# Optimization experiments

Hardware: AMD Instinct MI355X
Metric: run time of the kernel (lower is better)

Reference implementation:

```python
import jax, jax.numpy as jnp
import numpy as np

D = 1024


def setup_inputs() -> dict:
    key = jax.random.key(0)
    kx, kq, kk, kv, ko = jax.random.split(key, 5)
    scale = 0.02
    x = jax.random.normal(kx, (4, 2048, D), dtype=jnp.float32)
    Wq = jax.random.normal(kq, (D, D), dtype=jnp.float32) * scale
    Wk = jax.random.normal(kk, (D, D), dtype=jnp.float32) * scale
    Wv = jax.random.normal(kv, (D, D), dtype=jnp.float32) * scale
    Wo = jax.random.normal(ko, (D, D), dtype=jnp.float32) * scale
    return {"x": x, "Wq": Wq, "Wk": Wk, "Wv": Wv, "Wo": Wo}


def reference(x, Wq, Wk, Wv, Wo):
    # Linear projections (torch Linear: y = x @ W.T, no bias)
    q = jnp.einsum('bsd,ed->bse', x, Wq)
    k = jnp.einsum('bsd,ed->bse', x, Wk)
    v = jnp.einsum('bsd,ed->bse', x, Wv)
    d = x.shape[-1]
    # HRR binding: circular convolution of k and v along feature dim (rfft domain)
    Fk = jnp.fft.rfft(k, axis=-1)
    Fv = jnp.fft.rfft(v, axis=-1)
    Fq = jnp.fft.rfft(q, axis=-1)
    Fkv = Fk * Fv                      # bound key-value pairs, Fourier domain
    # causal cumulative memory over sequence; FFT is linear so cumsum commutes
    Fmem = jnp.cumsum(Fkv, axis=-2)    # [b, s, d//2+1] complex
    # unbind with query: circular correlation = multiply by conj(rfft(q))
    values_hat = jnp.fft.irfft(Fmem * jnp.conj(Fq), n=d, axis=-1)
    return jnp.einsum('bsd,ed->bse', values_hat, Wo)
```

## Files before the change

### kernel.cpp

```cpp
#include <hip/hip_runtime.h>
#include <hip/hip_fp16.h>

#define D_DIM 1024
#define NF 513
#define NB 4
#define NS 2048
#define NTOK (NB * NS)
#define NCH 32
#define CHS (NS / NCH)
#define NQKV 3200
#define KOUT 1088
#define USTRIDE 544

typedef __attribute__((ext_vector_type(8))) short short8_t;
typedef __attribute__((ext_vector_type(4))) float f32x4;

__device__ inline unsigned short f2bf(float f) {
    unsigned u = __builtin_bit_cast(unsigned, f);
    u += 0x7FFFu + ((u >> 16) & 1u);
    return (unsigned short)(u >> 16);
}
__device__ inline float bf2f(unsigned short h) {
    unsigned u = ((unsigned)h) << 16;
    return __builtin_bit_cast(float, u);
}
__device__ inline unsigned pkc(float re, float im) {
    return (unsigned)f2bf(re) | ((unsigned)f2bf(im) << 16);
}
__device__ inline float2 uph(unsigned u) {
    unsigned short lo = (unsigned short)(u & 0xFFFFu), hi = (unsigned short)(u >> 16);
    return make_float2(__half2float(__builtin_bit_cast(__half, lo)),
                       __half2float(__builtin_bit_cast(__half, hi)));
}

__global__ __launch_bounds__(256) void convert_x(const float* __restrict__ src,
                                                 unsigned short* __restrict__ dst,
                                                 int n4) {
    int i = blockIdx.x * 256 + threadIdx.x;
    int stride = gridDim.x * 256;
    for (; i < n4; i += stride) {
        float4 v = reinterpret_cast<const float4*>(src)[i];
        ushort4 o;
        o.x = f2bf(v.x); o.y = f2bf(v.y); o.z = f2bf(v.z); o.w = f2bf(v.w);
        reinterpret_cast<ushort4*>(dst)[i] = o;
    }
}

__device__ inline void gload_lds16(const void* g, void* l) {
    __builtin_amdgcn_global_load_lds(
        (const __attribute__((address_space(1))) void*)g,
        (__attribute__((address_space(3))) void*)l,
        16, 0, 0);
}

template <typename OutT, bool F16OUT>
__global__ __launch_bounds__(256) void gemm_bf16_bk64(const unsigned short* __restrict__ A,
                                                      const unsigned short* __restrict__ B,
                                                      OutT* __restrict__ C,
                                                      int M, int N, int K) {
    __shared__ __attribute__((aligned(16))) unsigned short ldsA[2 * 128 * 64];
    __shared__ __attribute__((aligned(16))) unsigned short ldsB[2 * 128 * 64];
    const int tid  = threadIdx.x;
    const int wave = tid >> 6;
    const int lane = tid & 63;
    const int l15  = lane & 15;
    const int q4   = (lane >> 4) & 3;
    const int h7   = l15 & 7;
    const int p0   = ((q4)     ^ h7) << 3;
    const int p1   = ((4 + q4) ^ h7) << 3;
    const int wm   = (wave >> 1) * 64;
    const int wn   = (wave & 1) * 64;
    const int bm   = blockIdx.x * 128;
    const int bn   = blockIdx.y * 128;
    const int srow = tid >> 3;
    const int scol = (((tid & 7) ^ ((tid >> 3) & 7)) << 3);
    const int NT   = K >> 6;

    const unsigned short* Asrc = A + (size_t)(bm + srow) * K + scol;
    const unsigned short* Bsrc = B + (size_t)(bn + srow) * K + scol;
    const size_t cstep = (size_t)32 * K;

    f32x4 acc[4][4];
#pragma unroll
    for (int i = 0; i < 4; ++i)
#pragma unroll
        for (int j = 0; j < 4; ++j)
            acc[i][j] = (f32x4){0.f, 0.f, 0.f, 0.f};

    auto STAGE = [&](int t, int b) {
        const int k0 = t << 6;
        unsigned short* la = &ldsA[b * 8192 + tid * 8];
        unsigned short* lb = &ldsB[b * 8192 + tid * 8];
        gload_lds16(Asrc + k0,             la);
        gload_lds16(Asrc + cstep + k0,     la + 2048);
        gload_lds16(Asrc + 2 * cstep + k0, la + 4096);
        gload_lds16(Asrc + 3 * cstep + k0, la + 6144);
        gload_lds16(Bsrc + k0,             lb);
        gload_lds16(Bsrc + cstep + k0,     lb + 2048);
        gload_lds16(Bsrc + 2 * cstep + k0, lb + 4096);
        gload_lds16(Bsrc + 3 * cstep + k0, lb + 6144);
    };

    STAGE(0, 0);

    for (int j = 0; j < NT; ++j) {
        const int buf = j & 1;
        if (j + 1 < NT) {
            STAGE(j + 1, buf ^ 1);
            asm volatile("s_waitcnt vmcnt(8)" ::: "memory");
        } else {
            asm volatile("s_waitcnt vmcnt(0)" ::: "memory");
        }
        __builtin_amdgcn_s_barrier();
        asm volatile("" ::: "memory");

        const unsigned short* la = &ldsA[buf * 8192];
        const unsigned short* lb = &ldsB[buf * 8192];

        {
            short8_t af[4], bfv[4];
#pragma unroll
            for (int mi = 0; mi < 4; ++mi)
                af[mi] = *reinterpret_cast<const short8_t*>(&la[(wm + mi * 16 + l15) * 64 + p0]);
#pragma unroll
            for (int ni = 0; ni < 4; ++ni)
                bfv[ni] = *reinterpret_cast<const short8_t*>(&lb[(wn + ni * 16 + l15) * 64 + p0]);
            __builtin_amdgcn_s_setprio(1);
#pragma unroll
            for (int mi = 0; mi < 4; ++mi)
#pragma unroll
                for (int ni = 0; ni < 4; ++ni)
                    acc[mi][ni] = __builtin_amdgcn_mfma_f32_16x16x32_bf16(af[mi], bfv[ni], acc[mi][ni], 0, 0, 0);
            __builtin_amdgcn_s_setprio(0);
        }
        {
            short8_t af[4], bfv[4];
#pragma unroll
            for (int mi = 0; mi < 4; ++mi)
                af[mi] = *reinterpret_cast<const short8_t*>(&la[(wm + mi * 16 + l15) * 64 + p1]);
#pragma unroll
            for (int ni = 0; ni < 4; ++ni)
                bfv[ni] = *reinterpret_cast<const short8_t*>(&lb[(wn + ni * 16 + l15) * 64 + p1]);
            __builtin_amdgcn_s_setprio(1);
#pragma unroll
            for (int mi = 0; mi < 4; ++mi)
#pragma unroll
                for (int ni = 0; ni < 4; ++ni)
                    acc[mi][ni] = __builtin_amdgcn_mfma_f32_16x16x32_bf16(af[mi], bfv[ni], acc[mi][ni], 0, 0, 0);
            __builtin_amdgcn_s_setprio(0);
        }

        __builtin_amdgcn_s_barrier();
        asm volatile("" ::: "memory");
    }

#pragma unroll
    for (int mi = 0; mi < 4; ++mi) {
        int rbase = bm + wm + mi * 16 + (lane >> 4) * 4;
#pragma unroll
        for (int ni = 0; ni < 4; ++ni) {
            int col = bn + wn + ni * 16 + l15;
#pragma unroll
            for (int j = 0; j < 4; ++j) {
                float v = acc[mi][ni][j];
                if constexpr (sizeof(OutT) == 4)
                    C[(size_t)(rbase + j) * N + col] = v;
                else if constexpr (F16OUT)
                    C[(size_t)(rbase + j) * N + col] =
                        __builtin_bit_cast(unsigned short, __float2half(v));
                else
                    C[(size_t)(rbase + j) * N + col] = f2bf(v);
            }
        }
    }
}

__device__ inline int sw(int i) { return i ^ ((i >> 4) & 15); }

__device__ inline int dr4(int n) {
    return ((n & 3) << 8) | (((n >> 2) & 3) << 6) | (((n >> 4) & 3) << 4) |
           (((n >> 6) & 3) << 2) | ((n >> 8) & 3);
}

__device__ inline float2 cmul(float2 a, float2 b) {
    return make_float2(a.x * b.x - a.y * b.y, a.x * b.y + a.y * b.x);
}

__device__ inline void fft1024_r4(float2* X, const float2* tw, int t) {
#pragma unroll
    for (int s = 0; s < 5; ++s) {
        const int L = 1 << (2 * s);
        const int r = t & (L - 1);
        const int base = ((t >> (2 * s)) << (2 * s + 2)) + r;
        float2 A  = X[sw(base)];
        float2 Bv = X[sw(base + L)];
        float2 Cv = X[sw(base + 2 * L)];
        float2 Dv = X[sw(base + 3 * L)];
        if (s != 0) {
            const int step = 1024 >> (2 * s + 2);
            Bv = cmul(Bv, tw[sw(r * step)]);
            Cv = cmul(Cv, tw[sw(2 * r * step)]);
            Dv = cmul(Dv, tw[sw(3 * r * step)]);
        }
        float2 e0 = make_float2(A.x + Cv.x, A.y + Cv.y);
        float2 e1 = make_float2(A.x - Cv.x, A.y - Cv.y);
        float2 o0 = make_float2(Bv.x + Dv.x, Bv.y + Dv.y);
        float2 o1 = make_float2(Bv.x - Dv.x, Bv.y - Dv.y);
        X[sw(base)]         = make_float2(e0.x + o0.x, e0.y + o0.y);
        X[sw(base + L)]     = make_float2(e1.x + o1.y, e1.y - o1.x);
        X[sw(base + 2 * L)] = make_float2(e0.x - o0.x, e0.y - o0.y);
        X[sw(base + 3 * L)] = make_float2(e1.x - o1.y, e1.y + o1.x);
        __syncthreads();
    }
}

__global__ __launch_bounds__(256) void twiddle_init(float2* __restrict__ twg) {
    int k = blockIdx.x * 256 + threadIdx.x;
    if (k < 768) {
        float ang = -6.283185307179586f * (float)k / 1024.0f;
        float s, c;
        sincosf(ang, &s, &c);
        twg[sw(k)] = make_float2(c, s);
    }
}

__global__ __launch_bounds__(256) void wf_qkv(const float* __restrict__ Wq,
                                              const float* __restrict__ Wk,
                                              const float* __restrict__ Wv,
                                              const float2* __restrict__ twg,
                                              unsigned short* __restrict__ WF) {
    __shared__ __attribute__((aligned(16))) float2 X[1024];
    __shared__ __attribute__((aligned(16))) float2 twL[768];
    const int tid = threadIdx.x;
    const int w = blockIdx.y;
    const float* W = (w == 0) ? Wq : (w == 1) ? Wk : Wv;
    const int d0 = blockIdx.x * 2;
    for (int i = tid; i < 384; i += 256)
        reinterpret_cast<float4*>(twL)[i] = reinterpret_cast<const float4*>(twg)[i];
    for (int n = tid; n < 1024; n += 256) {
        float2 z = *reinterpret_cast<const float2*>(W + (size_t)n * 1024 + d0);
        X[sw(dr4(n))] = z;
    }
    __syncthreads();
    fft1024_r4(X, twL, tid);
    const int rbase = w * 1026;
    for (int f = tid; f < NF; f += 256) {
        float2 Zj = X[sw(f)];
        float2 Zm = X[sw((1024 - f) & 1023)];
        float re0 = 0.5f * (Zj.x + Zm.x), im0 = 0.5f * (Zj.y - Zm.y);
        float re1 = 0.5f * (Zj.y + Zm.y), im1 = 0.5f * (Zm.x - Zj.x);
        WF[(size_t)(rbase + 2 * f)     * 1024 + d0]     = f2bf(re0);
        WF[(size_t)(rbase + 2 * f + 1) * 1024 + d0]     = f2bf(im0);
        WF[(size_t)(rbase + 2 * f)     * 1024 + d0 + 1] = f2bf(re1);
        WF[(size_t)(rbase + 2 * f + 1) * 1024 + d0 + 1] = f2bf(im1);
    }
}

__global__ __launch_bounds__(256) void wf_zero(unsigned* __restrict__ p) {
    int i = blockIdx.x * 256 + threadIdx.x;
    if (i < 62464) p[i] = 0;
}

__global__ __launch_bounds__(256) void wf_o(const float* __restrict__ Wo,
                                            const float2* __restrict__ twg,
                                            unsigned short* __restrict__ Wt) {
    __shared__ __attribute__((aligned(16))) float2 X[1024];
    __shared__ __attribute__((aligned(16))) float2 twL[768];
    const int tid = threadIdx.x;
    const int e0 = blockIdx.x * 2;
    for (int i = tid; i < 384; i += 256)
        reinterpret_cast<float4*>(twL)[i] = reinterpret_cast<const float4*>(twg)[i];
    const float* r0 = Wo + (size_t)e0 * 1024;
    const float* r1 = r0 + 1024;
    for (int n = tid; n < 1024; n += 256)
        X[sw(dr4(n))] = make_float2(r0[n], r1[n]);
    __syncthreads();
    fft1024_r4(X, twL, tid);
    unsigned short* o0 = Wt + (size_t)e0 * KOUT;
    unsigned short* o1 = o0 + KOUT;
    for (int f = tid; f < NF; f += 256) {
        float2 Zj = X[sw(f)];
        float2 Zm = X[sw((1024 - f) & 1023)];
        float c = (f == 0 || f == 512) ? (1.0f / 1024.0f) : (2.0f / 1024.0f);
        o0[2 * f]     = f2bf(0.5f * (Zj.x + Zm.x) * c);
        o0[2 * f + 1] = f2bf(0.5f * (Zj.y - Zm.y) * c);
        o1[2 * f]     = f2bf(0.5f * (Zj.y + Zm.y) * c);
        o1[2 * f + 1] = f2bf(0.5f * (Zm.x - Zj.x) * c);
    }
    for (int j = tid; j < KOUT - 2 * NF; j += 256) {
        o0[2 * NF + j] = 0;
        o1[2 * NF + j] = 0;
    }
}

__global__ __launch_bounds__(256) void hrr_chunk_sum(const unsigned* __restrict__ F,
                                                     float2* __restrict__ part) {
    int f = blockIdx.x * 256 + threadIdx.x;
    if (f >= NF) return;
    int ch = blockIdx.y, b = blockIdx.z;
    float sx = 0.f, sy = 0.f;
    size_t base = ((size_t)b * NS + (size_t)ch * CHS) * 1600;
    for (int i = 0; i < CHS; ++i) {
        size_t row = base + (size_t)i * 1600;
        float2 k = uph(F[row + 513 + f]);
        float2 v = uph(F[row + 1026 + f]);
        sx += k.x * v.x - k.y * v.y;
        sy += k.x * v.y + k.y * v.x;
    }
    part[(size_t)(b * NCH + ch) * NF + f] = make_float2(sx, sy);
}

__global__ __launch_bounds__(256) void hrr_scan_apply(const unsigned* __restrict__ F,
                                                      const float2* __restrict__ part,
                                                      unsigned* __restrict__ U) {
    int f = blockIdx.x * 256 + threadIdx.x;
    if (f >= USTRIDE) return;
    int ch = blockIdx.y, b = blockIdx.z;
    size_t ubase = ((size_t)b * NS + (size_t)ch * CHS) * USTRIDE + f;
    if (f >= NF) {
        for (int i = 0; i < CHS; ++i) U[ubase + (size_t)i * USTRIDE] = 0;
        return;
    }
    float rx = 0.f, ry = 0.f;
    for (int c2 = 0; c2 < ch; ++c2) {
        float2 p = part[(size_t)(b * NCH + c2) * NF + f];
        rx += p.x; ry += p.y;
    }
    size_t base = ((size_t)b * NS + (size_t)ch * CHS) * 1600;
    for (int i = 0; i < CHS; ++i) {
        size_t row = base + (size_t)i * 1600;
        float2 k = uph(F[row + 513 + f]);
        float2 v = uph(F[row + 1026 + f]);
        rx += k.x * v.x - k.y * v.y;
        ry += k.x * v.y + k.y * v.x;
        float2 q = uph(F[row + f]);
        U[ubase + (size_t)i * USTRIDE] = pkc(rx * q.x + ry * q.y,
                                            ry * q.x - rx * q.y);
    }
}

extern "C" void kernel_launch(void* const* d_in, const int* in_sizes, int n_in,
                              void* d_out, int out_size, void* d_ws, size_t ws_size,
                              hipStream_t stream) {
    const float* x  = (const float*)d_in[0];
    const float* Wq = (const float*)d_in[1];
    const float* Wk = (const float*)d_in[2];
    const float* Wv = (const float*)d_in[3];
    const float* Wo = (const float*)d_in[4];
    float* out = (float*)d_out;

    char* ws = (char*)d_ws;
    unsigned short* F_all = (unsigned short*)(ws + 0);
    unsigned short* U     = (unsigned short*)(ws + 52428800);
    float2*         part  = (float2*)        (ws + 70254592);
    float2*         twg   = (float2*)        (ws + 70779904);
    unsigned short* WF    = (unsigned short*)(ws + 70786048);
    unsigned short* Wt    = (unsigned short*)(ws + 77339648);
    unsigned short* xb    = (unsigned short*)(ws + 79567872);

    convert_x<<<2048, 256, 0, stream>>>(x, xb, NTOK * D_DIM / 4);
    twiddle_init<<<3, 256, 0, stream>>>(twg);

    wf_qkv<<<dim3(512, 3), 256, 0, stream>>>(Wq, Wk, Wv, twg, WF);
    wf_zero<<<244, 256, 0, stream>>>((unsigned*)(WF + (size_t)3078 * 1024));
    wf_o<<<512, 256, 0, stream>>>(Wo, twg, Wt);

    dim3 gq(NTOK / 128, NQKV / 128);
    gemm_bf16_bk64<unsigned short, true><<<gq, 256, 0, stream>>>(xb, WF, F_all, NTOK, NQKV, D_DIM);

    dim3 gs((USTRIDE + 255) / 256, NCH, NB);
    hrr_chunk_sum<<<dim3(3, NCH, NB), 256, 0, stream>>>((const unsigned*)F_all, part);
    hrr_scan_apply<<<gs, 256, 0, stream>>>((const unsigned*)F_all, part, (unsigned*)U);

    dim3 go(NTOK / 128, D_DIM / 128);
    gemm_bf16_bk64<float, false><<<go, 256, 0, stream>>>(U, Wt, out, NTOK, D_DIM, KOUT);
}
```

Measured before the change: 191.3 us.

## Pack DC and Nyquist real parts into one complex slot to drop spectrum padding

The real FFT spectrum is stored as 512 complex slots by packing the purely real DC and Nyquist coefficients into slot 0. This shrinks the QKV projection GEMM N dimension from 3200 to 3072 and the output GEMM K from 1088 to 1024, and removes the zero-padding kernels and padded columns. The HRR scan kernels special-case slot 0 so it handles two real accumulators. This cuts GEMM work and memory traffic by roughly 4-6% but adds branching for one thread per block.

```diff
diff --git a/kernel.cpp b/kernel.cpp
--- a/kernel.cpp
+++ b/kernel.cpp
@@ -8,9 +8,8 @@
 #define NTOK (NB * NS)
 #define NCH 32
 #define CHS (NS / NCH)
-#define NQKV 3200
-#define KOUT 1088
-#define USTRIDE 544
+#define NQKV 3072
+#define KOUT 1024
 
 typedef __attribute__((ext_vector_type(8))) short short8_t;
 typedef __attribute__((ext_vector_type(4))) float f32x4;
@@ -243,22 +242,25 @@
     }
     __syncthreads();
     fft1024_r4(X, twL, tid);
-    const int rbase = w * 1026;
+    const int rbase = w * 1024;
     for (int f = tid; f < NF; f += 256) {
         float2 Zj = X[sw(f)];
         float2 Zm = X[sw((1024 - f) & 1023)];
         float re0 = 0.5f * (Zj.x + Zm.x), im0 = 0.5f * (Zj.y - Zm.y);
         float re1 = 0.5f * (Zj.y + Zm.y), im1 = 0.5f * (Zm.x - Zj.x);
-        WF[(size_t)(rbase + 2 * f)     * 1024 + d0]     = f2bf(re0);
-        WF[(size_t)(rbase + 2 * f + 1) * 1024 + d0]     = f2bf(im0);
-        WF[(size_t)(rbase + 2 * f)     * 1024 + d0 + 1] = f2bf(re1);
-        WF[(size_t)(rbase + 2 * f + 1) * 1024 + d0 + 1] = f2bf(im1);
-    }
-}
-
-__global__ __launch_bounds__(256) void wf_zero(unsigned* __restrict__ p) {
-    int i = blockIdx.x * 256 + threadIdx.x;
-    if (i < 62464) p[i] = 0;
+        if (f == 0) {
+            WF[(size_t)(rbase + 0) * 1024 + d0]     = f2bf(re0);
+            WF[(size_t)(rbase + 0) * 1024 + d0 + 1] = f2bf(re1);
+        } else if (f == 512) {
+            WF[(size_t)(rbase + 1) * 1024 + d0]     = f2bf(re0);
+            WF[(size_t)(rbase + 1) * 1024 + d0 + 1] = f2bf(re1);
+        } else {
+            WF[(size_t)(rbase + 2 * f)     * 1024 + d0]     = f2bf(re0);
+            WF[(size_t)(rbase + 2 * f + 1) * 1024 + d0]     = f2bf(im0);
+            WF[(size_t)(rbase + 2 * f)     * 1024 + d0 + 1] = f2bf(re1);
+            WF[(size_t)(rbase + 2 * f + 1) * 1024 + d0 + 1] = f2bf(im1);
+        }
+    }
 }
 
 __global__ __launch_bounds__(256) void wf_o(const float* __restrict__ Wo,
@@ -278,64 +280,97 @@
     fft1024_r4(X, twL, tid);
     unsigned short* o0 = Wt + (size_t)e0 * KOUT;
     unsigned short* o1 = o0 + KOUT;
+    const float inv = 1.0f / 1024.0f;
     for (int f = tid; f < NF; f += 256) {
         float2 Zj = X[sw(f)];
         float2 Zm = X[sw((1024 - f) & 1023)];
-        float c = (f == 0 || f == 512) ? (1.0f / 1024.0f) : (2.0f / 1024.0f);
-        o0[2 * f]     = f2bf(0.5f * (Zj.x + Zm.x) * c);
-        o0[2 * f + 1] = f2bf(0.5f * (Zj.y - Zm.y) * c);
-        o1[2 * f]     = f2bf(0.5f * (Zj.y + Zm.y) * c);
-        o1[2 * f + 1] = f2bf(0.5f * (Zm.x - Zj.x) * c);
-    }
-    for (int j = tid; j < KOUT - 2 * NF; j += 256) {
-        o0[2 * NF + j] = 0;
-        o1[2 * NF + j] = 0;
+        float re0 = 0.5f * (Zj.x + Zm.x), im0 = 0.5f * (Zj.y - Zm.y);
+        float re1 = 0.5f * (Zj.y + Zm.y), im1 = 0.5f * (Zm.x - Zj.x);
+        if (f == 0) {
+            o0[0] = f2bf(re0 * inv);
+            o1[0] = f2bf(re1 * inv);
+        } else if (f == 512) {
+            o0[1] = f2bf(re0 * inv);
+            o1[1] = f2bf(re1 * inv);
+        } else {
+            float c = 2.0f * inv;
+            o0[2 * f]     = f2bf(re0 * c);
+            o0[2 * f + 1] = f2bf(im0 * c);
+            o1[2 * f]     = f2bf(re1 * c);
+            o1[2 * f + 1] = f2bf(im1 * c);
+        }
     }
 }
 
 __global__ __launch_bounds__(256) void hrr_chunk_sum(const unsigned* __restrict__ F,
                                                      float2* __restrict__ part) {
     int f = blockIdx.x * 256 + threadIdx.x;
-    if (f >= NF) return;
     int ch = blockIdx.y, b = blockIdx.z;
-    float sx = 0.f, sy = 0.f;
-    size_t base = ((size_t)b * NS + (size_t)ch * CHS) * 1600;
-    for (int i = 0; i < CHS; ++i) {
-        size_t row = base + (size_t)i * 1600;
-        float2 k = uph(F[row + 513 + f]);
-        float2 v = uph(F[row + 1026 + f]);
-        sx += k.x * v.x - k.y * v.y;
-        sy += k.x * v.y + k.y * v.x;
-    }
-    part[(size_t)(b * NCH + ch) * NF + f] = make_float2(sx, sy);
+    size_t base = ((size_t)b * NS + (size_t)ch * CHS) * 1536;
+    float2* pp = part + (size_t)(b * NCH + ch) * NF;
+    if (f == 0) {
+        float s0 = 0.f, s512 = 0.f;
+        for (int i = 0; i < CHS; ++i) {
+            size_t row = base + (size_t)i * 1536;
+            float2 k = uph(F[row + 512]);
+            float2 v = uph(F[row + 1024]);
+            s0   += k.x * v.x;
+            s512 += k.y * v.y;
+        }
+        pp[0]   = make_float2(s0, 0.f);
+        pp[512] = make_float2(s512, 0.f);
+    } else {
+        float sx = 0.f, sy = 0.f;
+        for (int i = 0; i < CHS; ++i) {
+            size_t row = base + (size_t)i * 1536;
+            float2 k = uph(F[row + 512 + f]);
+            float2 v = uph(F[row + 1024 + f]);
+            sx += k.x * v.x - k.y * v.y;
+            sy += k.x * v.y + k.y * v.x;
+        }
+        pp[f] = make_float2(sx, sy);
+    }
 }
 
 __global__ __launch_bounds__(256) void hrr_scan_apply(const unsigned* __restrict__ F,
                                                       const float2* __restrict__ part,
                                                       unsigned* __restrict__ U) {
     int f = blockIdx.x * 256 + threadIdx.x;
-    if (f >= USTRIDE) return;
     int ch = blockIdx.y, b = blockIdx.z;
-    size_t ubase = ((size_t)b * NS + (size_t)ch * CHS) * USTRIDE + f;
-    if (f >= NF) {
-        for (int i = 0; i < CHS; ++i) U[ubase + (size_t)i * USTRIDE] = 0;
-        return;
-    }
-    float rx = 0.f, ry = 0.f;
-    for (int c2 = 0; c2 < ch; ++c2) {
-        float2 p = part[(size_t)(b * NCH + c2) * NF + f];
-        rx += p.x; ry += p.y;
-    }
-    size_t base = ((size_t)b * NS + (size_t)ch * CHS) * 1600;
-    for (int i = 0; i < CHS; ++i) {
-        size_t row = base + (size_t)i * 1600;
-        float2 k = uph(F[row + 513 + f]);
-        float2 v = uph(F[row + 1026 + f]);
-        rx += k.x * v.x - k.y * v.y;
-        ry += k.x * v.y + k.y * v.x;
-        float2 q = uph(F[row + f]);
-        U[ubase + (size_t)i * USTRIDE] = pkc(rx * q.x + ry * q.y,
-                                            ry * q.x - rx * q.y);
+    size_t base  = ((size_t)b * NS + (size_t)ch * CHS) * 1536;
+    size_t ubase = ((size_t)b * NS + (size_t)ch * CHS) * 512;
+    const float2* pp = part + (size_t)b * NCH * NF;
+    if (f == 0) {
+        float r0 = 0.f, r512 = 0.f;
+        for (int c2 = 0; c2 < ch; ++c2) {
+            r0   += pp[(size_t)c2 * NF + 0].x;
+            r512 += pp[(size_t)c2 * NF + 512].x;
+        }
+        for (int i = 0; i < CHS; ++i) {
+            size_t row = base + (size_t)i * 1536;
+            float2 k = uph(F[row + 512]);
+            float2 v = uph(F[row + 1024]);
+            float2 q = uph(F[row]);
+            r0   += k.x * v.x;
+            r512 += k.y * v.y;
+            U[ubase + (size_t)i * 512] = pkc(r0 * q.x, r512 * q.y);
+        }
+    } else {
+        float rx = 0.f, ry = 0.f;
+        for (int c2 = 0; c2 < ch; ++c2) {
+            float2 p = pp[(size_t)c2 * NF + f];
+            rx += p.x; ry += p.y;
+        }
+        for (int i = 0; i < CHS; ++i) {
+            size_t row = base + (size_t)i * 1536;
+            float2 k = uph(F[row + 512 + f]);
+            float2 v = uph(F[row + 1024 + f]);
+            rx += k.x * v.x - k.y * v.y;
+            ry += k.x * v.y + k.y * v.x;
+            float2 q = uph(F[row + f]);
+            U[ubase + (size_t)i * 512 + f] = pkc(rx * q.x + ry * q.y,
+                                                 ry * q.x - rx * q.y);
+        }
     }
 }
 
@@ -351,25 +386,24 @@
 
     char* ws = (char*)d_ws;
     unsigned short* F_all = (unsigned short*)(ws + 0);
-    unsigned short* U     = (unsigned short*)(ws + 52428800);
-    float2*         part  = (float2*)        (ws + 70254592);
-    float2*         twg   = (float2*)        (ws + 70779904);
-    unsigned short* WF    = (unsigned short*)(ws + 70786048);
-    unsigned short* Wt    = (unsigned short*)(ws + 77339648);
-    unsigned short* xb    = (unsigned short*)(ws + 79567872);
+    unsigned short* U     = (unsigned short*)(ws + 50331648);
+    float2*         part  = (float2*)        (ws + 67108864);
+    float2*         twg   = (float2*)        (ws + 67634176);
+    unsigned short* WF    = (unsigned short*)(ws + 67640320);
+    unsigned short* Wt    = (unsigned short*)(ws + 73931776);
+    unsigned short* xb    = (unsigned short*)(ws + 76028928);
 
     convert_x<<<2048, 256, 0, stream>>>(x, xb, NTOK * D_DIM / 4);
     twiddle_init<<<3, 256, 0, stream>>>(twg);
 
     wf_qkv<<<dim3(512, 3), 256, 0, stream>>>(Wq, Wk, Wv, twg, WF);
-    wf_zero<<<244, 256, 0, stream>>>((unsigned*)(WF + (size_t)3078 * 1024));
     wf_o<<<512, 256, 0, stream>>>(Wo, twg, Wt);
 
     dim3 gq(NTOK / 128, NQKV / 128);
     gemm_bf16_bk64<unsigned short, true><<<gq, 256, 0, stream>>>(xb, WF, F_all, NTOK, NQKV, D_DIM);
 
-    dim3 gs((USTRIDE + 255) / 256, NCH, NB);
-    hrr_chunk_sum<<<dim3(3, NCH, NB), 256, 0, stream>>>((const unsigned*)F_all, part);
+    dim3 gs(2, NCH, NB);
+    hrr_chunk_sum<<<gs, 256, 0, stream>>>((const unsigned*)F_all, part);
     hrr_scan_apply<<<gs, 256, 0, stream>>>((const unsigned*)F_all, part, (unsigned*)U);
 
     dim3 go(NTOK / 128, D_DIM / 128);
```

After: 177.7 us. 7.1% less time.
